# Performance work log

Hardware: AMD Instinct MI355X
Metric: run time of the kernel (lower is better)

Reference implementation:

```python
import jax, jax.numpy as jnp
import numpy as np
from jax import lax

# --- static config (mirrors cfg / init args) ---
B, T, F_IN = 4, 1024, 80      # batch, time steps, mel bins (80 -> freq collapses to 1)
C_EMB = 512                   # cfg.dim_embed
C0 = C_EMB // 2               # first_conv_filters (non-tcn branch)
HEADS, K = 8, 7               # num_heads, NA kernel_size (dilation=1)
D_HEAD = C_EMB // HEADS
MLP = 4 * C_EMB               # mlp_ratio=4
EPS = 1e-5                    # layer_norm_eps


def setup_inputs() -> dict:
    key = jax.random.key(0)
    ks = jax.random.split(key, 16)
    rn = lambda k, s, sc=0.02: jax.random.normal(k, s, dtype=jnp.float32) * sc
    z = lambda *s: jnp.zeros(s, dtype=jnp.float32)
    o = lambda *s: jnp.ones(s, dtype=jnp.float32)
    return {
        "x": jax.random.normal(ks[0], (B, 1, T, F_IN), dtype=jnp.float32),
        # conv embedding stack (OIHW)
        "conv0_w": rn(ks[1], (C0, 1, 3, 3), 0.1), "conv0_b": z(C0),
        "conv1_w": rn(ks[2], (C_EMB, C0, 1, 12), 0.02), "conv1_b": z(C_EMB),
        "conv2_w": rn(ks[3], (C_EMB, C_EMB, 3, 3), 0.02), "conv2_b": z(C_EMB),
        "emb_ln_g": o(C_EMB), "emb_ln_b": z(C_EMB),
        # neighborhood attention (linear weights stored [in,out]; apply as x @ W + b)
        "q_w": rn(ks[4], (C_EMB, C_EMB)), "q_b": z(C_EMB),
        "k_w": rn(ks[5], (C_EMB, C_EMB)), "k_b": z(C_EMB),
        "v_w": rn(ks[6], (C_EMB, C_EMB)), "v_b": z(C_EMB),
        "rpb": rn(ks[7], (HEADS, 2 * K - 1)),
        "attn_out_w": rn(ks[8], (C_EMB, C_EMB)), "attn_out_b": z(C_EMB),
        "ln1_g": o(C_EMB), "ln1_b": z(C_EMB),
        "ln2_g": o(C_EMB), "ln2_b": z(C_EMB),
        "mlp1_w": rn(ks[9], (C_EMB, MLP)), "mlp1_b": z(MLP),
        "mlp2_w": rn(ks[10], (MLP, C_EMB)), "mlp2_b": z(C_EMB),
    }


def _layer_norm(x, g, b):
    m = jnp.mean(x, axis=-1, keepdims=True)
    v = jnp.mean(jnp.square(x - m), axis=-1, keepdims=True)
    return (x - m) * lax.rsqrt(v + EPS) * g + b


def _na1d(q, k, v, rpb):
    """1D neighborhood attention (natten1dqkrpb + softmax + natten1dav), dilation=1.
    q,k,v: [B,H,T,D]; rpb: [H,2K-1]. Returns [B,H,T,D]."""
    Bq, H, Tq, D = q.shape
    ni = jnp.clip(jnp.arange(Tq) - K // 2, 0, Tq - K)        # window start per query
    idx = ni[:, None] + jnp.arange(K)                         # [T,K] key positions
    k_win = k[:, :, idx]                                      # [B,H,T,K,D]
    v_win = v[:, :, idx]                                      # [B,H,T,K,D]
    scores = jnp.einsum('bhtd,bhtkd->bhtk', q, k_win)
    rel = idx - jnp.arange(Tq)[:, None] + (K - 1)             # [T,K] in [0,2K-2]
    scores = scores + rpb[:, rel][None]                       # + [1,H,T,K]
    probs = jax.nn.softmax(scores, axis=-1)
    return jnp.einsum('bhtk,bhtkd->bhtd', probs, v_win)


def _forward(x, conv0_w, conv0_b, conv1_w, conv1_b, conv2_w, conv2_b,
             emb_ln_g, emb_ln_b, q_w, q_b, k_w, k_b, v_w, v_b, rpb,
             attn_out_w, attn_out_b, ln1_g, ln1_b, ln2_g, ln2_b,
             mlp1_w, mlp1_b, mlp2_w, mlp2_b):
    conv = lambda h, w, b, pad: lax.conv_general_dilated(
        h, w, (1, 1), pad, dimension_numbers=('NCHW', 'OIHW', 'NCHW')
    ) + b[None, :, None, None]
    pool3 = lambda h: lax.reduce_window(h, -jnp.inf, lax.max,
                                        (1, 1, 1, 3), (1, 1, 1, 3), 'VALID')
    # --- AllInOneEmbeddings (eval: dropouts are no-ops) ---
    h = jax.nn.relu(pool3(conv(x, conv0_w, conv0_b, [(1, 1), (0, 0)])))
    h = jax.nn.relu(pool3(conv(h, conv1_w, conv1_b, [(0, 0), (0, 0)])))
    h = jax.nn.relu(pool3(conv(h, conv2_w, conv2_b, [(1, 1), (0, 0)])))
    h = jnp.transpose(h[..., 0], (0, 2, 1))                   # [B,T,C]
    emb = _layer_norm(h, emb_ln_g, emb_ln_b)
    # --- DinatLayer1d (double_attention=False, drop_path=0) ---
    Bh, Th, Ch = emb.shape
    shortcut = emb
    hs = _layer_norm(emb, ln1_g, ln1_b)
    heads = lambda y: jnp.transpose(y.reshape(Bh, Th, HEADS, D_HEAD), (0, 2, 1, 3))
    q = heads(hs @ q_w + q_b) * (1.0 / jnp.sqrt(jnp.float32(D_HEAD)))
    kk = heads(hs @ k_w + k_b)
    vv = heads(hs @ v_w + v_b)
    ctx = _na1d(q, kk, vv, rpb)                               # [B,H,T,D]
    ctx = jnp.transpose(ctx, (0, 2, 1, 3)).reshape(Bh, Th, Ch)
    attn = ctx @ attn_out_w + attn_out_b                      # NeighborhoodAttentionOutput
    hs = shortcut + attn
    ln = _layer_norm(hs, ln2_g, ln2_b)
    mlp = jax.nn.gelu(ln @ mlp1_w + mlp1_b, approximate=False) @ mlp2_w + mlp2_b
    return hs + mlp


def reference(x, conv0_w, conv0_b, conv1_w, conv1_b, conv2_w, conv2_b,
              emb_ln_g, emb_ln_b, q_w, q_b, k_w, k_b, v_w, v_b, rpb,
              attn_out_w, attn_out_b, ln1_g, ln1_b, ln2_g, ln2_b,
              mlp1_w, mlp1_b, mlp2_w, mlp2_b):
    return _forward(x, conv0_w, conv0_b, conv1_w, conv1_b, conv2_w, conv2_b,
                    emb_ln_g, emb_ln_b, q_w, q_b, k_w, k_b, v_w, v_b, rpb,
                    attn_out_w, attn_out_b, ln1_g, ln1_b, ln2_g, ln2_b,
                    mlp1_w, mlp1_b, mlp2_w, mlp2_b)
```

## Files before the change

### kernel.cpp

```cpp
#include <hip/hip_runtime.h>
#include <hip/hip_bf16.h>
#include <math.h>


typedef __bf16 bf16x8 __attribute__((ext_vector_type(8)));
typedef float f32x4 __attribute__((ext_vector_type(4)));

static __device__ __forceinline__ short f2bf(float f) {
  __hip_bfloat16 h = __float2bfloat16(f);
  return __builtin_bit_cast(short, h);
}

static __device__ __forceinline__ float wave_sum(float v) {
#pragma unroll
  for (int o = 32; o; o >>= 1) v += __shfl_xor(v, o);
  return v;
}

static __device__ __forceinline__ void gld16(const void* g, void* l) {
  __builtin_amdgcn_global_load_lds(
      (const __attribute__((address_space(1))) unsigned int*)g,
      (__attribute__((address_space(3))) unsigned int*)l, 16, 0, 0);
}

__global__ __launch_bounds__(256) void conv0_kernel(
    const float* __restrict__ x, const float* __restrict__ w,
    const float* __restrict__ bias, short* __restrict__ h0) {
  const int b = blockIdx.x >> 10;
  const int t = blockIdx.x & 1023;
  const int c = threadIdx.x;
  __shared__ float xs[3][80];
  for (int i = threadIdx.x; i < 240; i += 256) {
    int dt = i / 80, f = i - dt * 80;
    int tt = t + dt - 1;
    xs[dt][f] = (tt >= 0 && tt < 1024) ? x[(b * 1024 + tt) * 80 + f] : 0.f;
  }
  float wr[9];
#pragma unroll
  for (int i = 0; i < 9; ++i) wr[i] = w[c * 9 + i];
  const float bi = bias[c];
  __syncthreads();
  const int cc = c >> 5, q = (c >> 3) & 3, e = c & 7;
  short* outb = &h0[((size_t)(b * 8 + cc) * 1024 + t) * 896];
  for (int fo = 0; fo < 26; ++fo) {
    float m = -1e30f;
#pragma unroll
    for (int p = 0; p < 3; ++p) {
      const int f = fo * 3 + p;
      float acc = bi;
#pragma unroll
      for (int dt = 0; dt < 3; ++dt)
#pragma unroll
        for (int df = 0; df < 3; ++df)
          acc += xs[dt][f + df] * wr[dt * 3 + df];
      m = fmaxf(m, acc);
    }
    const int row = t * 28 + fo;
    outb[fo * 32 + (q ^ ((row >> 1) & 3)) * 8 + e] = f2bf(fmaxf(m, 0.f));
  }
  if (c < 64) outb[832 + c] = 0;
}

__global__ __launch_bounds__(256) void prep_w1(const float* __restrict__ w,
                                               short* __restrict__ wt) {
  const int co = blockIdx.x;
  __shared__ float ls[3072];
  for (int i = threadIdx.x; i < 3072; i += 256) ls[i] = w[co * 3072 + i];
  __syncthreads();
  const int swz = (co >> 1) & 3;
  for (int i = threadIdx.x; i < 3072; i += 256) {
    const int e = i & 7, q = (i >> 3) & 3, kw = (i >> 5) % 12, cc = i / 384;
    const int ci = cc * 32 + q * 8 + e;
    wt[(((size_t)(cc * 12 + kw) * 512 + co) * 4 + (q ^ swz)) * 8 + e] =
        f2bf(ls[ci * 12 + kw]);
  }
}

__global__ __launch_bounds__(256) void prep_w2(const float* __restrict__ w,
                                               short* __restrict__ wt) {
  const int co = blockIdx.x;
  __shared__ float ls[4608];
  for (int i = threadIdx.x; i < 4608; i += 256) ls[i] = w[co * 4608 + i];
  __syncthreads();
  const int swz = (co >> 1) & 3;
  for (int i = threadIdx.x; i < 4608; i += 256) {
    const int e = i & 7, q = (i >> 3) & 3, p = (i >> 5) % 9, cc = i / 288;
    const int ci = cc * 32 + q * 8 + e;
    wt[(((size_t)(cc * 9 + p) * 512 + co) * 4 + (q ^ swz)) * 8 + e] =
        f2bf(ls[ci * 9 + p]);
  }
}

__global__ __launch_bounds__(256) void prep_all(
    const float* __restrict__ q_w, const float* __restrict__ k_w,
    const float* __restrict__ v_w, const float* __restrict__ ao_w,
    const float* __restrict__ m1_w, const float* __restrict__ m2_w,
    const float* __restrict__ q_b, const float* __restrict__ k_b,
    const float* __restrict__ v_b,
    short* __restrict__ wtqkv, short* __restrict__ wtao,
    short* __restrict__ wtm1, short* __restrict__ wtm2,
    float* __restrict__ qkvb, short* __restrict__ h1) {
  const int g = blockIdx.x;
  if (g < 3072) {
    const float* src; short* dst; int K, N, t0;
    if (g < 256)       { src = q_w;  dst = wtqkv;             K = 512;  N = 512;  t0 = g; }
    else if (g < 512)  { src = k_w;  dst = wtqkv + 512 * 512; K = 512;  N = 512;  t0 = g - 256; }
    else if (g < 768)  { src = v_w;  dst = wtqkv + 1024 * 512; K = 512; N = 512;  t0 = g - 512; }
    else if (g < 1024) { src = ao_w; dst = wtao;              K = 512;  N = 512;  t0 = g - 768; }
    else if (g < 2048) { src = m1_w; dst = wtm1;              K = 512;  N = 2048; t0 = g - 1024; }
    else               { src = m2_w; dst = wtm2;              K = 2048; N = 512;  t0 = g - 2048; }
    const int ntn = N >> 5;
    const int kt = t0 / ntn, nt = t0 - kt * ntn;
    const int k0 = kt * 32, n0 = nt * 32;
    __shared__ float tile[32][33];
    const int tx = threadIdx.x & 31, ty = threadIdx.x >> 5;
    for (int r = ty; r < 32; r += 8)
      tile[r][tx] = src[(size_t)(k0 + r) * N + n0 + tx];
    __syncthreads();
    for (int r = ty; r < 32; r += 8)
      dst[(size_t)(n0 + r) * K + k0 + tx] = f2bf(tile[tx][r]);
  } else if (g < 3136) {
    short* base = h1 + (size_t)(g - 3072) * 164160;
    for (int i = threadIdx.x; i < 160; i += 256) {
      base[i] = 0;
      base[1025 * 160 + i] = 0;
    }
  } else {
    const int i = (g - 3136) * 256 + threadIdx.x;
    qkvb[i] = i < 512 ? q_b[i] : (i < 1024 ? k_b[i - 512] : v_b[i - 1024]);
  }
}

__global__ __launch_bounds__(512) void conv1_kernel(
    const short* __restrict__ h0, const short* __restrict__ wt1,
    const float* __restrict__ bias, short* __restrict__ h1) {
  const int b = blockIdx.x >> 5;
  const int t0 = (blockIdx.x & 31) * 32;
  const int co0 = blockIdx.y * 128;
  __shared__ short XsF[2][28672];
  __shared__ short AsF[2][8192];
  const int tid = threadIdx.x;
  const int lane = tid & 63;
  const int wid = tid >> 6;
  const int wm = wid >> 2;
  const int wn = wid & 3;
  const int l15 = lane & 15, lg = lane >> 4;

  const f32x4 zf = {0.f, 0.f, 0.f, 0.f};
  f32x4 acc[4][8];
#pragma unroll
  for (int i = 0; i < 4; ++i)
#pragma unroll
    for (int j = 0; j < 8; ++j) acc[i][j] = zf;

  auto stageX = [&](int cc, int buf) {
    const short* xs = h0 + ((size_t)(b * 8 + cc) * 1024 + t0) * 896;
#pragma unroll
    for (int i = 0; i < 7; ++i) {
      const int v = wid * 7 + i;
      gld16(xs + v * 512 + lane * 8, &XsF[buf][v * 512]);
    }
  };
  auto stageA = [&](int cc, int g, int buf) {
#pragma unroll
    for (int i = 0; i < 2; ++i) {
      const int u = wid * 2 + i;
      const int kwl = u >> 3, r = u & 7;
      gld16(wt1 + ((size_t)((cc * 12 + g * 2 + kwl) * 512) + co0) * 32 +
                r * 512 + lane * 8,
            &AsF[buf][kwl * 4096 + r * 512]);
    }
  };

  stageX(0, 0);
  stageA(0, 0, 0);
  asm volatile("s_waitcnt vmcnt(0)" ::: "memory");
  __builtin_amdgcn_s_barrier();

  for (int s = 0; s < 48; ++s) {
    const int cc = s / 6, g = s - cc * 6;
    if (s < 47) {
      const int s1 = s + 1;
      const int cc1 = s1 / 6, g1 = s1 - cc1 * 6;
      stageA(cc1, g1, s1 & 1);
      if (g1 == 0) {
        stageX(cc1, cc1 & 1);
        asm volatile("s_waitcnt vmcnt(9)" ::: "memory");
      } else {
        asm volatile("s_waitcnt vmcnt(2)" ::: "memory");
      }
    } else {
      asm volatile("s_waitcnt vmcnt(0)" ::: "memory");
    }
    __builtin_amdgcn_s_barrier();
    const short* Xb = XsF[cc & 1];
    const short* Ab = AsF[s & 1];
#pragma unroll
    for (int j = 0; j < 2; ++j) {
      const int kw = g * 2 + j;
      bf16x8 a[4];
#pragma unroll
      for (int sm = 0; sm < 4; ++sm) {
        const int co_l = wm * 64 + sm * 16 + l15;
        a[sm] = *reinterpret_cast<const bf16x8*>(
            &Ab[(j * 512 + co_l * 4 + (lg ^ ((co_l >> 1) & 3))) * 8]);
      }
#pragma unroll
      for (int sn = 0; sn < 8; ++sn) {
        const int row = (wn * 8 + sn) * 28 + l15 + kw;
        bf16x8 bf = *reinterpret_cast<const bf16x8*>(
            &Xb[(row * 4 + (lg ^ ((row >> 1) & 3))) * 8]);
#pragma unroll
        for (int sm = 0; sm < 4; ++sm)
          acc[sm][sn] = __builtin_amdgcn_mfma_f32_16x16x32_bf16(a[sm], bf, acc[sm][sn], 0, 0, 0);
      }
    }
    asm volatile("" ::: "memory");
    __builtin_amdgcn_s_barrier();
  }
  const int basel = lane & 48;
  const int wsrc = (l15 < 5) ? 3 * l15 : 0;
#pragma unroll
  for (int sm = 0; sm < 4; ++sm)
#pragma unroll
    for (int sn = 0; sn < 8; ++sn) {
      const int t = t0 + wn * 8 + sn;
#pragma unroll
      for (int r = 0; r < 4; ++r) {
        float val = acc[sm][sn][r];
        float v0 = __shfl(val, basel + wsrc);
        float v1 = __shfl(val, basel + wsrc + 1);
        float v2 = __shfl(val, basel + wsrc + 2);
        if (l15 < 5) {
          const int co = co0 + wm * 64 + sm * 16 + lg * 4 + r;
          float p = fmaxf(fmaxf(v0, v1), v2) + bias[co];
          const int cc2 = co >> 5, q = (co >> 3) & 3, e = co & 7;
          const int row_g = (t + 1) * 5 + l15;
          h1[((size_t)(b * 16 + cc2) * 1026 + (t + 1)) * 160 + l15 * 32 +
             (q ^ ((row_g >> 1) & 3)) * 8 + e] = f2bf(fmaxf(p, 0.f));
        }
      }
    }
}

__global__ __launch_bounds__(512) void conv2_kernel(
    const short* __restrict__ h1, const short* __restrict__ wt2,
    const float* __restrict__ bias, float* __restrict__ emb_in) {
  const int b = blockIdx.x >> 5;
  const int t0 = (blockIdx.x & 31) * 32;
  const int co0 = blockIdx.y * 128;
  __shared__ __align__(16) short smem2[35840];
  const int tid = threadIdx.x;
  const int lane = tid & 63;
  const int wid = tid >> 6;
  const int wm = wid >> 1;
  const int wn = wid & 1;
  const int l15 = lane & 15, lg = lane >> 4;
  const f32x4 zf = {0.f, 0.f, 0.f, 0.f};
  f32x4 acc[2][3];
#pragma unroll
  for (int i = 0; i < 2; ++i)
#pragma unroll
    for (int j = 0; j < 3; ++j) acc[i][j] = zf;
  int tl[3], dwl[3];
#pragma unroll
  for (int sn = 0; sn < 3; ++sn) {
    const int c = wn * 48 + sn * 16 + l15;
    tl[sn] = c / 3;
    dwl[sn] = c - tl[sn] * 3;
  }

  auto stageX = [&](int cc, int buf) {
    const short* xs = h1 + ((size_t)(b * 16 + cc) * 1026 + t0) * 160;
#pragma unroll
    for (int i = 0; i < 2; ++i) {
      const int v = wid + 8 * i;
      if (v < 11) gld16(xs + v * 512 + lane * 8, &smem2[buf * 5632 + v * 512]);
    }
  };
  auto stageA = [&](int cc, int g, int buf) {
#pragma unroll
    for (int i = 0; i < 3; ++i) {
      const int u = wid * 3 + i;
      const int pl = u >> 3, r = u & 7;
      gld16(wt2 + ((size_t)((cc * 9 + g * 3 + pl) * 512) + co0) * 32 +
                r * 512 + lane * 8,
            &smem2[11264 + buf * 12288 + pl * 4096 + r * 512]);
    }
  };

  stageX(0, 0);
  stageA(0, 0, 0);
  asm volatile("s_waitcnt vmcnt(0)" ::: "memory");
  __builtin_amdgcn_s_barrier();

  for (int s = 0; s < 48; ++s) {
    const int cc = s / 3, g = s - cc * 3;
    if (s < 47) {
      const int s1 = s + 1;
      const int cc1 = s1 / 3, g1 = s1 - cc1 * 3;
      stageA(cc1, g1, s1 & 1);
      if (g1 == 0) {
        stageX(cc1, cc1 & 1);
        if (wid < 3) asm volatile("s_waitcnt vmcnt(5)" ::: "memory");
        else         asm volatile("s_waitcnt vmcnt(4)" ::: "memory");
      } else {
        asm volatile("s_waitcnt vmcnt(3)" ::: "memory");
      }
    } else {
      asm volatile("s_waitcnt vmcnt(0)" ::: "memory");
    }
    __builtin_amdgcn_s_barrier();
    const short* Xb = &smem2[(cc & 1) * 5632];
    const short* Ab = &smem2[11264 + (s & 1) * 12288];
#pragma unroll
    for (int j = 0; j < 3; ++j) {
      bf16x8 a[2];
#pragma unroll
      for (int sm = 0; sm < 2; ++sm) {
        const int co_l = wm * 32 + sm * 16 + l15;
        a[sm] = *reinterpret_cast<const bf16x8*>(
            &Ab[(j * 512 + co_l * 4 + (lg ^ ((co_l >> 1) & 3))) * 8]);
      }
#pragma unroll
      for (int sn = 0; sn < 3; ++sn) {
        const int row = (tl[sn] + g) * 5 + dwl[sn] + j;
        bf16x8 xv = *reinterpret_cast<const bf16x8*>(
            &Xb[(row * 4 + (lg ^ ((row >> 1) & 3))) * 8]);
#pragma unroll
        for (int sm = 0; sm < 2; ++sm)
          acc[sm][sn] = __builtin_amdgcn_mfma_f32_16x16x32_bf16(a[sm], xv, acc[sm][sn], 0, 0, 0);
      }
    }
    asm volatile("" ::: "memory");
    __builtin_amdgcn_s_barrier();
  }
  float(*Ds)[100] = reinterpret_cast<float(*)[100]>(smem2);
#pragma unroll
  for (int sm = 0; sm < 2; ++sm)
#pragma unroll
    for (int sn = 0; sn < 3; ++sn)
#pragma unroll
      for (int r = 0; r < 4; ++r)
        Ds[wm * 32 + sm * 16 + lg * 4 + r][wn * 48 + sn * 16 + l15] = acc[sm][sn][r];
  __syncthreads();
  for (int e = tid; e < 4096; e += 512) {
    const int co = e & 127, tt = e >> 7;
    float m = fmaxf(fmaxf(Ds[co][tt * 3], Ds[co][tt * 3 + 1]), Ds[co][tt * 3 + 2]) + bias[co0 + co];
    emb_in[((size_t)(b * 1024) + t0 + tt) * 512 + co0 + co] = fmaxf(m, 0.f);
  }
}

__global__ __launch_bounds__(256) void ln_double_kernel(
    const float* __restrict__ x, const float* __restrict__ g0,
    const float* __restrict__ b0, const float* __restrict__ g1,
    const float* __restrict__ b1, float* __restrict__ o0, short* __restrict__ o1) {
  const int row = blockIdx.x * 4 + (threadIdx.x >> 6);
  const int lane = threadIdx.x & 63;
  const float* xr = x + (size_t)row * 512;
  float v[8];
#pragma unroll
  for (int j = 0; j < 8; ++j) v[j] = xr[j * 64 + lane];
  float s = 0;
#pragma unroll
  for (int j = 0; j < 8; ++j) s += v[j];
  s = wave_sum(s);
  const float mean = s * (1.f / 512.f);
  float q = 0;
#pragma unroll
  for (int j = 0; j < 8; ++j) { float d = v[j] - mean; q += d * d; }
  q = wave_sum(q);
  const float rs = rsqrtf(q * (1.f / 512.f) + 1e-5f);
#pragma unroll
  for (int j = 0; j < 8; ++j) {
    const int ci = j * 64 + lane;
    float e = (v[j] - mean) * rs * g0[ci] + b0[ci];
    o0[(size_t)row * 512 + ci] = e;
    v[j] = e;
  }
  s = 0;
#pragma unroll
  for (int j = 0; j < 8; ++j) s += v[j];
  s = wave_sum(s);
  const float mean2 = s * (1.f / 512.f);
  q = 0;
#pragma unroll
  for (int j = 0; j < 8; ++j) { float d = v[j] - mean2; q += d * d; }
  q = wave_sum(q);
  const float rs2 = rsqrtf(q * (1.f / 512.f) + 1e-5f);
#pragma unroll
  for (int j = 0; j < 8; ++j) {
    const int ci = j * 64 + lane;
    o1[(size_t)row * 512 + ci] = f2bf((v[j] - mean2) * rs2 * g1[ci] + b1[ci]);
  }
}

__global__ __launch_bounds__(256) void ln_kernel(
    const float* __restrict__ x, const float* __restrict__ g,
    const float* __restrict__ b, short* __restrict__ o) {
  const int row = blockIdx.x * 4 + (threadIdx.x >> 6);
  const int lane = threadIdx.x & 63;
  const float* xr = x + (size_t)row * 512;
  float v[8];
#pragma unroll
  for (int j = 0; j < 8; ++j) v[j] = xr[j * 64 + lane];
  float s = 0;
#pragma unroll
  for (int j = 0; j < 8; ++j) s += v[j];
  s = wave_sum(s);
  const float mean = s * (1.f / 512.f);
  float q = 0;
#pragma unroll
  for (int j = 0; j < 8; ++j) { float d = v[j] - mean; q += d * d; }
  q = wave_sum(q);
  const float rs = rsqrtf(q * (1.f / 512.f) + 1e-5f);
#pragma unroll
  for (int j = 0; j < 8; ++j) {
    const int ci = j * 64 + lane;
    o[(size_t)row * 512 + ci] = f2bf((v[j] - mean) * rs * g[ci] + b[ci]);
  }
}

__global__ __launch_bounds__(256) void na1d_kernel(
    const float* __restrict__ qkv, const float* __restrict__ rpb,
    short* __restrict__ ctx) {
  const int W = blockIdx.x * 4 + (threadIdx.x >> 6);
  const int lane = threadIdx.x & 63;
  const int b = W >> 13, h = (W >> 10) & 7, t = W & 1023;
  int ni = t - 3;
  ni = ni < 0 ? 0 : (ni > 1017 ? 1017 : ni);
  const float qv = qkv[((size_t)(b * 1024) + t) * 1536 + h * 64 + lane];
  const float* kb = qkv + 512 + ((size_t)(b * 1024) + ni) * 1536 + h * 64;
  float s[7];
#pragma unroll
  for (int j = 0; j < 7; ++j) {
    float pd = qv * kb[j * 1536 + lane];
    pd = wave_sum(pd);
    s[j] = pd + rpb[h * 13 + (ni + j - t + 6)];
  }
  float mx = s[0];
#pragma unroll
  for (int j = 1; j < 7; ++j) mx = fmaxf(mx, s[j]);
  float den = 0;
#pragma unroll
  for (int j = 0; j < 7; ++j) { s[j] = expf(s[j] - mx); den += s[j]; }
  const float inv = 1.f / den;
  const float* vb = qkv + 1024 + ((size_t)(b * 1024) + ni) * 1536 + h * 64;
  float o = 0;
#pragma unroll
  for (int j = 0; j < 7; ++j) o += s[j] * vb[j * 1536 + lane];
  ctx[((size_t)(b * 1024) + t) * 512 + h * 64 + lane] = f2bf(o * inv);
}

template <int EPI>
__global__ __launch_bounds__(256) void gemm_bf(
    const short* __restrict__ A, const short* __restrict__ Wt,
    const float* __restrict__ bias, const float* __restrict__ res,
    void* __restrict__ Cv, int K, int N) {
  const int m0 = blockIdx.x * 128, n0 = blockIdx.y * 64;
  __shared__ short Asm[2][8192];
  __shared__ short Bsm[2][4096];
  const int tid = threadIdx.x;
  const int wid = tid >> 6, lane = tid & 63;
  const int wm = wid >> 1, wn = wid & 1;
  const int l15 = lane & 15, lg = lane >> 4;
  const int srow = lane >> 3, su = lane & 7;
  const int ssw = (su ^ srow) << 3;
  const f32x4 zf = {0.f, 0.f, 0.f, 0.f};
  f32x4 acc[4][2];
#pragma unroll
  for (int i = 0; i < 4; ++i) { acc[i][0] = zf; acc[i][1] = zf; }

  auto stage = [&](int k0, int buf) {
#pragma unroll
    for (int i = 0; i < 4; ++i) {
      const int r0 = (wid * 4 + i) * 8;
      gld16(A + (size_t)(m0 + r0 + srow) * K + k0 + ssw, &Asm[buf][r0 * 64]);
    }
#pragma unroll
    for (int i = 0; i < 2; ++i) {
      const int r0 = (wid * 2 + i) * 8;
      gld16(Wt + (size_t)(n0 + r0 + srow) * K + k0 + ssw, &Bsm[buf][r0 * 64]);
    }
  };

  const int S = K >> 6;
  stage(0, 0);
  asm volatile("s_waitcnt vmcnt(0)" ::: "memory");
  __builtin_amdgcn_s_barrier();

  for (int s = 0; s < S; ++s) {
    if (s < S - 1) {
      stage((s + 1) << 6, (s + 1) & 1);
      asm volatile("s_waitcnt vmcnt(6)" ::: "memory");
    } else {
      asm volatile("s_waitcnt vmcnt(0)" ::: "memory");
    }
    __builtin_amdgcn_s_barrier();
    const short* Ab = Asm[s & 1];
    const short* Bb = Bsm[s & 1];
#pragma unroll
    for (int kk = 0; kk < 2; ++kk) {
      const int u = kk * 4 + lg;
      bf16x8 bfr[2];
#pragma unroll
      for (int sn = 0; sn < 2; ++sn) {
        const int rn = wn * 32 + sn * 16 + l15;
        bfr[sn] = *reinterpret_cast<const bf16x8*>(&Bb[rn * 64 + ((u ^ (rn & 7)) << 3)]);
      }
#pragma unroll
      for (int sm = 0; sm < 4; ++sm) {
        const int rm = wm * 64 + sm * 16 + l15;
        bf16x8 a = *reinterpret_cast<const bf16x8*>(&Ab[rm * 64 + ((u ^ (rm & 7)) << 3)]);
#pragma unroll
        for (int sn = 0; sn < 2; ++sn)
          acc[sm][sn] = __builtin_amdgcn_mfma_f32_16x16x32_bf16(a, bfr[sn], acc[sm][sn], 0, 0, 0);
      }
    }
    asm volatile("" ::: "memory");
    __builtin_amdgcn_s_barrier();
  }
#pragma unroll
  for (int sm = 0; sm < 4; ++sm)
#pragma unroll
    for (int sn = 0; sn < 2; ++sn)
#pragma unroll
      for (int r = 0; r < 4; ++r) {
        const int m = m0 + wm * 64 + sm * 16 + lg * 4 + r;
        const int n = n0 + wn * 32 + sn * 16 + l15;
        float val = acc[sm][sn][r] + bias[n];
        if (EPI == 2) {
          val = 0.5f * val * (1.f + erff(val * 0.70710678f));
          ((short*)Cv)[(size_t)m * N + n] = f2bf(val);
        } else {
          if (EPI == 3) val += res[(size_t)m * N + n];
          if (EPI == 4 && n < 512) val *= 0.125f;
          ((float*)Cv)[(size_t)m * N + n] = val;
        }
      }
}

extern "C" void kernel_launch(void* const* d_in, const int* in_sizes, int n_in,
                              void* d_out, int out_size, void* d_ws, size_t ws_size,
                              hipStream_t stream) {
  (void)in_sizes; (void)n_in; (void)out_size;
  const float* x        = (const float*)d_in[0];
  const float* conv0_w  = (const float*)d_in[1];
  const float* conv0_b  = (const float*)d_in[2];
  const float* conv1_w  = (const float*)d_in[3];
  const float* conv1_b  = (const float*)d_in[4];
  const float* conv2_w  = (const float*)d_in[5];
  const float* conv2_b  = (const float*)d_in[6];
  const float* emb_ln_g = (const float*)d_in[7];
  const float* emb_ln_b = (const float*)d_in[8];
  const float* q_w  = (const float*)d_in[9];
  const float* q_b  = (const float*)d_in[10];
  const float* k_w  = (const float*)d_in[11];
  const float* k_b  = (const float*)d_in[12];
  const float* v_w  = (const float*)d_in[13];
  const float* v_b  = (const float*)d_in[14];
  const float* rpb  = (const float*)d_in[15];
  const float* ao_w = (const float*)d_in[16];
  const float* ao_b = (const float*)d_in[17];
  const float* ln1_g = (const float*)d_in[18];
  const float* ln1_b = (const float*)d_in[19];
  const float* ln2_g = (const float*)d_in[20];
  const float* ln2_b = (const float*)d_in[21];
  const float* m1_w = (const float*)d_in[22];
  const float* m1_b = (const float*)d_in[23];
  const float* m2_w = (const float*)d_in[24];
  const float* m2_b = (const float*)d_in[25];

  char* ws = (char*)d_ws;
  size_t off = 0;
  auto alloc = [&](size_t bytes) -> char* {
    char* p = ws + off;
    off += (bytes + 255) & ~(size_t)255;
    return p;
  };
  short* h0   = (short*)alloc(4ull * 8 * 1024 * 896 * 2);
  short* h1   = (short*)alloc(4ull * 16 * 1026 * 160 * 2);
  float* embi = (float*)alloc(4ull * 1024 * 512 * 4);
  float* emb  = (float*)alloc(4ull * 1024 * 512 * 4);
  short* hs1  = (short*)alloc(4ull * 1024 * 512 * 2);
  float* qkv  = (float*)alloc(4ull * 1024 * 1536 * 4);
  short* ctx  = (short*)alloc(4ull * 1024 * 512 * 2);
  float* hs   = (float*)alloc(4ull * 1024 * 512 * 4);
  short* wt1  = (short*)alloc(512ull * 12 * 256 * 2);
  short* wt2  = (short*)alloc(512ull * 9 * 512 * 2);
  short* wtqkv = (short*)alloc(1536ull * 512 * 2);
  short* wtao = (short*)alloc(512ull * 512 * 2);
  short* wtm1 = (short*)alloc(2048ull * 512 * 2);
  short* wtm2 = (short*)alloc(512ull * 2048 * 2);
  float* qkvb = (float*)alloc(1536ull * 4);
  if (ws_size < off) return;
  short* mid  = (short*)h0;
  short* ln2o = (short*)embi;
  float* outp = (float*)d_out;

  prep_w1<<<512, 256, 0, stream>>>(conv1_w, wt1);
  prep_w2<<<512, 256, 0, stream>>>(conv2_w, wt2);
  prep_all<<<3142, 256, 0, stream>>>(q_w, k_w, v_w, ao_w, m1_w, m2_w,
                                     q_b, k_b, v_b,
                                     wtqkv, wtao, wtm1, wtm2, qkvb, h1);

  conv0_kernel<<<4096, 256, 0, stream>>>(x, conv0_w, conv0_b, h0);
  conv1_kernel<<<dim3(128, 4), 512, 0, stream>>>(h0, wt1, conv1_b, h1);
  conv2_kernel<<<dim3(128, 4), 512, 0, stream>>>(h1, wt2, conv2_b, embi);
  ln_double_kernel<<<1024, 256, 0, stream>>>(embi, emb_ln_g, emb_ln_b, ln1_g, ln1_b, emb, hs1);
  gemm_bf<4><<<dim3(32, 24), 256, 0, stream>>>(hs1, wtqkv, qkvb, nullptr, qkv, 512, 1536);
  na1d_kernel<<<8192, 256, 0, stream>>>(qkv, rpb, ctx);
  gemm_bf<3><<<dim3(32, 8), 256, 0, stream>>>(ctx, wtao, ao_b, emb, hs, 512, 512);
  ln_kernel<<<1024, 256, 0, stream>>>(hs, ln2_g, ln2_b, ln2o);
  gemm_bf<2><<<dim3(32, 32), 256, 0, stream>>>(ln2o, wtm1, m1_b, nullptr, mid, 512, 2048);
  gemm_bf<3><<<dim3(32, 8), 256, 0, stream>>>(mid, wtm2, m2_b, hs, outp, 2048, 512);
}
```

Measured before the change: 402.7 us.

## Restructure conv1 into smaller blocks with triple-buffered weight prefetch

```diff
diff --git a/kernel.cpp b/kernel.cpp
--- a/kernel.cpp
+++ b/kernel.cpp
@@ -131,19 +131,19 @@
   }
 }
 
-__global__ __launch_bounds__(512) void conv1_kernel(
+__global__ __launch_bounds__(256) void conv1_kernel(
     const short* __restrict__ h0, const short* __restrict__ wt1,
     const float* __restrict__ bias, short* __restrict__ h1) {
-  const int b = blockIdx.x >> 5;
-  const int t0 = (blockIdx.x & 31) * 32;
+  const int b = blockIdx.x >> 6;
+  const int t0 = (blockIdx.x & 63) * 16;
   const int co0 = blockIdx.y * 128;
-  __shared__ short XsF[2][28672];
-  __shared__ short AsF[2][8192];
+  __shared__ short Xs[2][14336];
+  __shared__ short As[3][4096];
   const int tid = threadIdx.x;
   const int lane = tid & 63;
   const int wid = tid >> 6;
-  const int wm = wid >> 2;
-  const int wn = wid & 3;
+  const int wm = wid >> 1;
+  const int wn = wid & 1;
   const int l15 = lane & 15, lg = lane >> 4;
 
   const f32x4 zf = {0.f, 0.f, 0.f, 0.f};
@@ -158,65 +158,65 @@
 #pragma unroll
     for (int i = 0; i < 7; ++i) {
       const int v = wid * 7 + i;
-      gld16(xs + v * 512 + lane * 8, &XsF[buf][v * 512]);
+      gld16(xs + v * 512 + lane * 8, &Xs[buf][v * 512]);
     }
   };
-  auto stageA = [&](int cc, int g, int buf) {
+  auto stageA = [&](int cc, int kw, int slot) {
 #pragma unroll
     for (int i = 0; i < 2; ++i) {
-      const int u = wid * 2 + i;
-      const int kwl = u >> 3, r = u & 7;
-      gld16(wt1 + ((size_t)((cc * 12 + g * 2 + kwl) * 512) + co0) * 32 +
-                r * 512 + lane * 8,
-            &AsF[buf][kwl * 4096 + r * 512]);
+      const int r = wid * 2 + i;
+      gld16(wt1 + ((size_t)((cc * 12 + kw) * 512) + co0) * 32 + r * 512 + lane * 8,
+            &As[slot][r * 512]);
     }
   };
 
   stageX(0, 0);
   stageA(0, 0, 0);
+  stageA(0, 1, 1);
   asm volatile("s_waitcnt vmcnt(0)" ::: "memory");
   __builtin_amdgcn_s_barrier();
 
-  for (int s = 0; s < 48; ++s) {
-    const int cc = s / 6, g = s - cc * 6;
-    if (s < 47) {
-      const int s1 = s + 1;
-      const int cc1 = s1 / 6, g1 = s1 - cc1 * 6;
-      stageA(cc1, g1, s1 & 1);
-      if (g1 == 0) {
-        stageX(cc1, cc1 & 1);
-        asm volatile("s_waitcnt vmcnt(9)" ::: "memory");
-      } else {
-        asm volatile("s_waitcnt vmcnt(2)" ::: "memory");
-      }
-    } else {
-      asm volatile("s_waitcnt vmcnt(0)" ::: "memory");
-    }
-    __builtin_amdgcn_s_barrier();
-    const short* Xb = XsF[cc & 1];
-    const short* Ab = AsF[s & 1];
-#pragma unroll
-    for (int j = 0; j < 2; ++j) {
-      const int kw = g * 2 + j;
-      bf16x8 a[4];
+  for (int cc = 0; cc < 8; ++cc) {
+    for (int kw = 0; kw < 12; ++kw) {
+      const short* Ab = As[kw % 3];
+      const short* Xb = Xs[cc & 1];
+      bf16x8 a[4], xv[8];
 #pragma unroll
       for (int sm = 0; sm < 4; ++sm) {
         const int co_l = wm * 64 + sm * 16 + l15;
         a[sm] = *reinterpret_cast<const bf16x8*>(
-            &Ab[(j * 512 + co_l * 4 + (lg ^ ((co_l >> 1) & 3))) * 8]);
+            &Ab[(co_l * 4 + (lg ^ ((co_l >> 1) & 3))) * 8]);
       }
 #pragma unroll
       for (int sn = 0; sn < 8; ++sn) {
         const int row = (wn * 8 + sn) * 28 + l15 + kw;
-        bf16x8 bf = *reinterpret_cast<const bf16x8*>(
+        xv[sn] = *reinterpret_cast<const bf16x8*>(
             &Xb[(row * 4 + (lg ^ ((row >> 1) & 3))) * 8]);
+      }
+      if (kw < 10) {
+        stageA(cc, kw + 2, (kw + 2) % 3);
+      } else if (cc < 7) {
+        stageA(cc + 1, kw - 10, (kw - 10) % 3);
+      }
+      if (kw == 0 && cc < 7) stageX(cc + 1, (cc + 1) & 1);
+      if (cc < 7 && kw <= 1) {
+        asm volatile("s_waitcnt vmcnt(9)" ::: "memory");
+      } else if (cc == 7 && kw >= 10) {
+        asm volatile("s_waitcnt vmcnt(0)" ::: "memory");
+      } else {
+        asm volatile("s_waitcnt vmcnt(2)" ::: "memory");
+      }
+      __builtin_amdgcn_s_barrier();
+      __builtin_amdgcn_s_setprio(1);
+#pragma unroll
+      for (int sn = 0; sn < 8; ++sn)
 #pragma unroll
         for (int sm = 0; sm < 4; ++sm)
-          acc[sm][sn] = __builtin_amdgcn_mfma_f32_16x16x32_bf16(a[sm], bf, acc[sm][sn], 0, 0, 0);
-      }
-    }
-    asm volatile("" ::: "memory");
-    __builtin_amdgcn_s_barrier();
+          acc[sm][sn] = __builtin_amdgcn_mfma_f32_16x16x32_bf16(a[sm], xv[sn], acc[sm][sn], 0, 0, 0);
+      __builtin_amdgcn_s_setprio(0);
+      asm volatile("" ::: "memory");
+      __builtin_amdgcn_s_barrier();
+    }
   }
   const int basel = lane & 48;
   const int wsrc = (l15 < 5) ? 3 * l15 : 0;
@@ -605,7 +605,7 @@
                                      wtqkv, wtao, wtm1, wtm2, qkvb, h1);
 
   conv0_kernel<<<4096, 256, 0, stream>>>(x, conv0_w, conv0_b, h0);
-  conv1_kernel<<<dim3(128, 4), 512, 0, stream>>>(h0, wt1, conv1_b, h1);
+  conv1_kernel<<<dim3(256, 4), 256, 0, stream>>>(h0, wt1, conv1_b, h1);
   conv2_kernel<<<dim3(128, 4), 512, 0, stream>>>(h1, wt2, conv2_b, embi);
   ln_double_kernel<<<1024, 256, 0, stream>>>(embi, emb_ln_g, emb_ln_b, ln1_g, ln1_b, emb, hs1);
   gemm_bf<4><<<dim3(32, 24), 256, 0, stream>>>(hs1, wtqkv, qkvb, nullptr, qkv, 512, 1536);
```

Result: slower. 518.1 us (+28.6%).
